# Performance work log

Hardware: AMD Instinct MI355X
Metric: run time of the kernel (lower is better)

Reference implementation:

```python
import jax, jax.numpy as jnp
import numpy as np

B, DX, DY = 128, 3, 3
D = DX * DY          # max_digit = 9
N = D * D            # num_nodes = 81
HID = 96
EMB = 16
ITERS = 4
M = B * N * D        # LSTM flattened rows = 93312


def _sudoku_adj():
    idx = np.arange(N)
    r, c = idx // D, idx % D
    br, bc = r // DX, c // DY
    same = (r[:, None] == r[None]) | (c[:, None] == c[None]) | ((br[:, None] == br[None]) & (bc[:, None] == bc[None]))
    return (same & ~np.eye(N, dtype=bool)).astype(np.float32)


def setup_inputs() -> dict:
    key = jax.random.key(0)
    ks = iter(jax.random.split(key, 40))

    def dense(shape, fan_in):
        return jax.random.normal(next(ks), shape, jnp.float32) / np.float32(np.sqrt(fan_in))

    return {
        "inputs": jax.random.randint(next(ks), (B, N), 0, D + 1, jnp.int32),
        "c0": jax.random.normal(next(ks), (M, HID), jnp.float32),
        "adj_cell": jnp.asarray((np.ones((D, D)) - np.eye(D)).astype(np.float32)),
        "adj_digit": jnp.asarray(_sudoku_adj()),
        "enc_W1": dense((3, EMB), 3), "enc_b1": jnp.zeros((EMB,), jnp.float32),
        "enc_W2": dense((EMB, HID), EMB), "enc_b2": jnp.zeros((HID,), jnp.float32),
        "cr_W": dense((3, HID, HID), HID), "cr_b": jnp.zeros((3, HID), jnp.float32),
        "dr_W": dense((3, HID, HID), HID), "dr_b": jnp.zeros((3, HID), jnp.float32),
        "gm_W1": dense((3 * HID, HID), 3 * HID), "gm_b1": jnp.zeros((HID,), jnp.float32),
        "gm_W2": dense((2, HID, HID), HID), "gm_b2": jnp.zeros((2, HID), jnp.float32),
        "lstm_Wih": dense((4 * HID, HID), HID), "lstm_Whh": dense((4 * HID, HID), HID),
        "lstm_bih": jnp.zeros((4 * HID,), jnp.float32), "lstm_bhh": jnp.zeros((4 * HID,), jnp.float32),
        "r_W12": dense((2, HID, HID), HID), "r_b12": jnp.zeros((2, HID), jnp.float32),
        "r_W3": dense((HID, 1), HID), "r_b3": jnp.zeros((1,), jnp.float32),
        "iters": ITERS,
    }


def _mlp(x, Ws, bs):
    # stacked MLP: ReLU between layers, none after the last
    L = Ws.shape[0]
    for l in range(L):
        x = x @ Ws[l] + bs[l]
        if l < L - 1:
            x = jax.nn.relu(x)
    return x


def _forward(inputs, c0, adj_cell, adj_digit, enc_W1, enc_b1, enc_W2, enc_b2,
             cr_W, cr_b, dr_W, dr_b, gm_W1, gm_b1, gm_W2, gm_b2,
             lstm_Wih, lstm_Whh, lstm_bih, lstm_bhh, r_W12, r_b12, r_W3, r_b3, iters):
    # mask: [B,N,D,3] = (blank, equals digit d+1, filled-with-other-digit)
    eq = inputs[:, :, None] == jnp.arange(1, D + 1, dtype=inputs.dtype)[None, None, :]
    given = inputs != 0
    mask = jnp.stack([
        jnp.broadcast_to((~given)[:, :, None], eq.shape), eq,
        (~eq) & given[:, :, None]
    ], axis=-1).astype(jnp.float32)

    X = jax.nn.relu(mask @ enc_W1 + enc_b1) @ enc_W2 + enc_b2  # [B,N,D,HID]

    def lstm_step(x, h, c):
        gates = x @ lstm_Wih.T + lstm_bih + h @ lstm_Whh.T + lstm_bhh
        i, f, g, o = jnp.split(gates, 4, axis=-1)  # PyTorch gate order i,f,g,o
        c = jax.nn.sigmoid(f) * c + jax.nn.sigmoid(i) * jnp.tanh(g)
        h = jax.nn.sigmoid(o) * jnp.tanh(c)
        return h, c

    def step(carry, _):
        h, c = carry  # [M,HID] each
        Hn = h.reshape(X.shape)
        # relational message passing: per-node MLP then sum over graph edges
        msg_cell = jnp.einsum('bndh,de->bneh', _mlp(Hn, cr_W, cr_b), adj_cell)
        msg_digit = jnp.einsum('bndh,nm->bmdh', _mlp(Hn, dr_W, dr_b), adj_digit)
        g = jnp.concatenate([X, msg_cell, msg_digit], axis=-1)  # [B,N,D,3*HID]
        g = jax.nn.relu(g @ gm_W1 + gm_b1)
        g = jax.nn.relu(g @ gm_W2[0] + gm_b2[0])
        g = g @ gm_W2[1] + gm_b2[1]
        h, c = lstm_step(g.reshape(-1, HID), h, c)
        Hn = h.reshape(X.shape)
        out = jax.nn.relu(Hn @ r_W12[0] + r_b12[0])
        out = jax.nn.relu(out @ r_W12[1] + r_b12[1])
        out = (out @ r_W3 + r_b3)[..., 0]  # [B,N,D]
        return (h, c), out

    (_, _), outs = jax.lax.scan(step, (X.reshape(-1, HID), c0), None, length=iters)
    return outs  # [iters,B,N,D]


def reference(inputs, c0, adj_cell, adj_digit, enc_W1, enc_b1, enc_W2, enc_b2,
              cr_W, cr_b, dr_W, dr_b, gm_W1, gm_b1, gm_W2, gm_b2,
              lstm_Wih, lstm_Whh, lstm_bih, lstm_bhh, r_W12, r_b12, r_W3, r_b3, iters):
    return _forward(inputs, c0, adj_cell, adj_digit, enc_W1, enc_b1, enc_W2, enc_b2,
                    cr_W, cr_b, dr_W, dr_b, gm_W1, gm_b1, gm_W2, gm_b2,
                    lstm_Wih, lstm_Whh, lstm_bih, lstm_bhh, r_W12, r_b12, r_W3, r_b3, iters)
```

## Files before the change

kernel.cpp:

```cpp
#include <hip/hip_runtime.h>
#include <hip/hip_bf16.h>

typedef unsigned short u16;
typedef __bf16 bf16x8 __attribute__((ext_vector_type(8)));
typedef float  f32x4  __attribute__((ext_vector_type(4)));
typedef u16    u16x8  __attribute__((ext_vector_type(8)));

#define HID   96
#define LDP   104
#define MROWS 93312
#define BN    10368
#define GRID_TILE 1458
#define FUSE_GRID 5832
#define SGX   100
#define PST   97
#define TBUF  1664
#define FST   520

#define FCH 9216

#define MFMA(a,b,c) __builtin_amdgcn_mfma_f32_16x16x32_bf16((a),(b),(c),0,0,0)

__device__ __forceinline__ float bf2f(u16 x){
  union { float f; unsigned u; } v; v.u = ((unsigned)x) << 16; return v.f;
}
__device__ __forceinline__ u16 f2bf(float f){
  union { __bf16 b; u16 u; } v; v.b = (__bf16)f; return v.u;
}
__device__ __forceinline__ float frcp(float x){ return __builtin_amdgcn_rcpf(x); }
__device__ __forceinline__ float sigf(float x){ return frcp(1.f + __expf(-x)); }
__device__ __forceinline__ float tanhf_(float x){
  float xx = fminf(fmaxf(x, -15.f), 15.f);
  float e = __expf(-2.f * xx);
  return (1.f - e) * frcp(1.f + e);
}
__device__ __forceinline__ void lds_fence(){
  asm volatile("s_waitcnt lgkmcnt(0)" ::: "memory");
}

struct Frags { bf16x8 a0, a1, a2; };

__device__ __forceinline__ Frags load_afrags_g(const u16* __restrict__ A, size_t row0, int lane){
  int t16 = lane & 15, q = lane >> 4;
  const u16* p = A + (row0 + (size_t)t16) * 96 + q * 8;
  Frags f;
  f.a0 = *reinterpret_cast<const bf16x8*>(p);
  f.a1 = *reinterpret_cast<const bf16x8*>(p + 32);
  f.a2 = *reinterpret_cast<const bf16x8*>(p + 64);
  return f;
}
__device__ __forceinline__ Frags load_afrags_s(const u16* sA, int row0, int lane){
  int t16 = lane & 15, q = lane >> 4;
  const u16* p = sA + (row0 + t16) * LDP + q * 8;
  Frags f;
  f.a0 = *reinterpret_cast<const bf16x8*>(p);
  f.a1 = *reinterpret_cast<const bf16x8*>(p + 32);
  f.a2 = *reinterpret_cast<const bf16x8*>(p + 64);
  return f;
}

__device__ __forceinline__ void layer_g(Frags f, const u16* __restrict__ wb,
    const float* __restrict__ bias, u16* dst, int dstStride, size_t rowBase,
    bool relu, int lane)
{
  int t16 = lane & 15, q = lane >> 4;
  #pragma unroll
  for (int nt = 0; nt < 6; nt++){
    float b = bias ? bias[nt * 16 + t16] : 0.f;
    f32x4 acc = {b, b, b, b};
    const u16* wp = wb + nt * 1536 + lane * 8;
    acc = MFMA(f.a0, *reinterpret_cast<const bf16x8*>(wp),        acc);
    acc = MFMA(f.a1, *reinterpret_cast<const bf16x8*>(wp + 512),  acc);
    acc = MFMA(f.a2, *reinterpret_cast<const bf16x8*>(wp + 1024), acc);
    #pragma unroll
    for (int j = 0; j < 4; j++){
      float v = acc[j];
      if (relu) v = fmaxf(v, 0.f);
      dst[(rowBase + q * 4 + j) * (size_t)dstStride + nt * 16 + t16] = f2bf(v);
    }
  }
}

__device__ __forceinline__ void layer_split(Frags f, const u16* __restrict__ wb,
    const float* __restrict__ bias, u16* dst, bool relu, int lane, int w)
{
  int t16 = lane & 15, q = lane >> 4;
  #pragma unroll
  for (int nt = w; nt < 6; nt += 4){
    float b = bias ? bias[nt * 16 + t16] : 0.f;
    f32x4 acc = {b, b, b, b};
    const u16* wp = wb + nt * 1536 + lane * 8;
    acc = MFMA(f.a0, *reinterpret_cast<const bf16x8*>(wp),        acc);
    acc = MFMA(f.a1, *reinterpret_cast<const bf16x8*>(wp + 512),  acc);
    acc = MFMA(f.a2, *reinterpret_cast<const bf16x8*>(wp + 1024), acc);
    #pragma unroll
    for (int j = 0; j < 4; j++){
      float v = acc[j];
      if (relu) v = fmaxf(v, 0.f);
      dst[(q * 4 + j) * LDP + nt * 16 + t16] = f2bf(v);
    }
  }
}

__device__ __forceinline__ void mfma6_g(f32x4* acc, Frags f,
    const u16* __restrict__ wb, int lane)
{
  #pragma unroll
  for (int jt = 0; jt < 6; jt++){
    const u16* wp = wb + jt * 1536 + lane * 8;
    acc[jt] = MFMA(f.a0, *reinterpret_cast<const bf16x8*>(wp),        acc[jt]);
    acc[jt] = MFMA(f.a1, *reinterpret_cast<const bf16x8*>(wp + 512),  acc[jt]);
    acc[jt] = MFMA(f.a2, *reinterpret_cast<const bf16x8*>(wp + 1024), acc[jt]);
  }
}

__global__ __launch_bounds__(256) void k_prep2(const float* __restrict__ crW,
    const float* __restrict__ drW, const float* __restrict__ gmW2,
    const float* __restrict__ rW12, const float* __restrict__ Whh,
    u16* __restrict__ pWB)
{
  int b = blockIdx.x, tid = threadIdx.x;
  if (b < 7){
    const float* src; int ch;
    if      (b == 0){ src = crW;          ch = 0;  }
    else if (b == 1){ src = crW  + 9216;  ch = 1;  }
    else if (b == 2){ src = drW;          ch = 3;  }
    else if (b == 3){ src = drW  + 9216;  ch = 4;  }
    else if (b == 4){ src = gmW2;         ch = 8;  }
    else if (b == 5){ src = rW12;         ch = 10; }
    else            { src = rW12 + 9216;  ch = 11; }
    u16* dst = pWB + ch * FCH;
    #pragma unroll
    for (int i = 0; i < 36; i++){
      int idx = tid + i * 256;
      int f = idx >> 9, rem = idx & 511, l = rem >> 3, j = rem & 7;
      int nt = f / 3, kc = f - nt * 3;
      int n = nt * 16 + (l & 15);
      int k = ((l >> 4) << 3) + kc * 32 + j;
      dst[idx] = f2bf(src[k * 96 + n]);
    }
  } else {
    int bb = b - 7;
    u16* dst = pWB + (16 + bb) * FCH;
    const float* src = Whh + bb * 9216;
    #pragma unroll
    for (int i = 0; i < 36; i++){
      int idx = tid + i * 256;
      int f = idx >> 9, rem = idx & 511, l = rem >> 3, j = rem & 7;
      int nt = f / 3, kc = f - nt * 3;
      int n = nt * 16 + (l & 15);
      int k = ((l >> 4) << 3) + kc * 32 + j;
      dst[idx] = f2bf(src[n * 96 + k]);
    }
  }
}

__global__ __launch_bounds__(256) void k_prepadj(u16* __restrict__ adjM)
{
  int tid = threadIdx.x;
  for (int i = tid; i < 9216; i += 256){
    int m = i / 96, n = i - (i / 96) * 96;
    float v = 0.f;
    if (m < 81 && n < 81 && m != n){
      int rm = m / 9, cm = m - rm * 9;
      int rn = n / 9, cn = n - rn * 9;
      if (rm == rn || cm == cn || ((rm / 3 == rn / 3) && (cm / 3 == cn / 3)))
        v = 1.f;
    }
    adjM[i] = f2bf(v);
  }
}

__global__ __launch_bounds__(256) void k_prepc(const float* __restrict__ crW,
    const float* __restrict__ crB, const float* __restrict__ drW,
    const float* __restrict__ drB, const float* __restrict__ gmW1,
    u16* __restrict__ pWB, float* __restrict__ bY, float* __restrict__ bZ)
{
  __shared__ float sM[96 * PST];
  __shared__ float sW[96 * PST];
  int b = blockIdx.x, g = b / 9, seg = b - g * 9, tid = threadIdx.x;
  const float* L = (g == 0 ? crW : drW) + 2 * 9216;
  const float* R = gmW1 + (g == 0 ? 9216 : 18432);
  for (int i = tid; i < 9216; i += 256){
    int r = i / 96, cc = i - r * 96;
    sM[r * PST + cc] = L[i];
    sW[r * PST + cc] = R[i];
  }
  __syncthreads();
  if (seg == 0){
    const float* bv = (g == 0 ? crB : drB) + 192;
    float* bo = (g == 0 ? bY : bZ);
    for (int n = tid; n < 96; n += 256){
      float a = 0.f;
      for (int j = 0; j < 96; j++) a += bv[j] * sW[j * PST + n];
      bo[n] = a;
    }
  }
  u16* dst = pWB + (g == 0 ? 2 : 5) * FCH;
  #pragma unroll
  for (int i = 0; i < 4; i++){
    int idx = seg * 1024 + tid + i * 256;
    int f = idx >> 9, rem = idx & 511, l = rem >> 3, j = rem & 7;
    int nt = f / 3, kc = f - nt * 3;
    int n = nt * 16 + (l & 15);
    int k = ((l >> 4) << 3) + kc * 32 + j;
    float a = 0.f;
    #pragma unroll 4
    for (int jj = 0; jj < 96; jj++) a += sM[k * PST + jj] * sW[jj * PST + n];
    dst[idx] = f2bf(a);
  }
}

__global__ __launch_bounds__(256) void k_prepf(const float* __restrict__ gmW2,
    const float* __restrict__ Wih, u16* __restrict__ pWB)
{
  __shared__ float sW[96 * PST];
  int b = blockIdx.x, g = b / 9, seg = b - g * 9, tid = threadIdx.x;
  for (int i = tid; i < 9216; i += 256){
    int r = i / 96, cc = i - r * 96;
    sW[r * PST + cc] = gmW2[9216 + i];
  }
  __syncthreads();
  u16* dst = pWB + (12 + g) * FCH;
  #pragma unroll
  for (int i = 0; i < 4; i++){
    int idx = seg * 1024 + tid + i * 256;
    int f = idx >> 9, rem = idx & 511, l = rem >> 3, j = rem & 7;
    int nt = f / 3, kc = f - nt * 3;
    int n = nt * 16 + (l & 15);
    int k = ((l >> 4) << 3) + kc * 32 + j;
    const float* wr = Wih + (g * 96 + n) * 96;
    float a = 0.f;
    #pragma unroll 4
    for (int jj = 0; jj < 96; jj++) a += sW[k * PST + jj] * wr[jj];
    dst[idx] = f2bf(a);
  }
}

__global__ void k_tables(const float* __restrict__ eW1, const float* __restrict__ eb1,
                         const float* __restrict__ eW2, const float* __restrict__ eb2,
                         const float* __restrict__ gmW1, const float* __restrict__ gmb1,
                         const float* __restrict__ bih, const float* __restrict__ bhh,
                         const float* __restrict__ gmb2, const float* __restrict__ Wih,
                         float* __restrict__ XTab, float* __restrict__ XgTab,
                         float* __restrict__ bsx)
{
  __shared__ float sX[3][96];
  int j = threadIdx.x;
  for (int n = j; n < 384; n += 128){
    float acc = bih[n] + bhh[n];
    const float* wr = Wih + n * 96;
    for (int jj = 0; jj < 96; jj++) acc += gmb2[96 + jj] * wr[jj];
    bsx[n] = acc;
  }
  if (j < 96){
    for (int ch = 0; ch < 3; ch++){
      float acc = eb2[j];
      for (int e = 0; e < 16; e++){
        float hv = fmaxf(eW1[ch * 16 + e] + eb1[e], 0.f);
        acc += hv * eW2[e * 96 + j];
      }
      sX[ch][j] = acc;
      XTab[ch * 96 + j] = acc;
    }
  }
  __syncthreads();
  if (j < 96){
    for (int ch = 0; ch < 3; ch++){
      float acc = gmb1[j];
      for (int k = 0; k < 96; k++) acc += sX[ch][k] * gmW1[k * 96 + j];
      XgTab[ch * 96 + j] = acc;
    }
  }
}

__global__ __launch_bounds__(256) void k_init(const int* __restrict__ inputs,
    const float* __restrict__ XTab, u16* __restrict__ h)
{
  int idx = blockIdx.x * 256 + threadIdx.x;
  int m = idx / 12, h8 = idx - m * 12;
  int bn = m / 9, d = m - bn * 9;
  int inp = inputs[bn];
  int ch = (inp == 0) ? 0 : ((inp == d + 1) ? 1 : 2);
  const float* xt = XTab + ch * 96 + h8 * 8;
  u16* hp = h + (size_t)m * 96 + h8 * 8;
  #pragma unroll
  for (int e = 0; e < 8; e++) hp[e] = f2bf(xt[e]);
}

__global__ __launch_bounds__(256) void k_ab3(const u16* __restrict__ h,
    u16* __restrict__ Y, u16* __restrict__ Z,
    const u16* __restrict__ pWB, const float* __restrict__ crB,
    const float* __restrict__ drB, const float* __restrict__ bY,
    const float* __restrict__ bZ)
{
  __shared__ u16 sA[64 * LDP];
  const int tid = threadIdx.x, lane = tid & 63, wave = tid >> 6;
  const int wrow = wave * 16;
  const size_t rbase = (size_t)blockIdx.x * 64;

  Frags hf = load_afrags_g(h, rbase + wrow, lane);

  layer_g(hf, pWB, crB, sA, LDP, wrow, true, lane);                  lds_fence();
  Frags f = load_afrags_s(sA, wrow, lane);
  layer_g(f, pWB + 1 * FCH, crB + 96, sA, LDP, wrow, true, lane);    lds_fence();
  f = load_afrags_s(sA, wrow, lane);
  layer_g(f, pWB + 2 * FCH, bY, Y, 96, rbase + wrow, false, lane);
  lds_fence();

  layer_g(hf, pWB + 3 * FCH, drB, sA, LDP, wrow, true, lane);        lds_fence();
  f = load_afrags_s(sA, wrow, lane);
  layer_g(f, pWB + 4 * FCH, drB + 96, sA, LDP, wrow, true, lane);    lds_fence();
  f = load_afrags_s(sA, wrow, lane);
  layer_g(f, pWB + 5 * FCH, bZ, Z, 96, rbase + wrow, false, lane);
}

__global__ __launch_bounds__(256) void k_msg(u16* __restrict__ Z,
    const u16* __restrict__ Y, u16* __restrict__ Ssum,
    const u16* __restrict__ adjM)
{
  __shared__ u16 sF[18 * FST];
  const int tid = threadIdx.x;
  if (blockIdx.x >= 1152){
    int idx = (blockIdx.x - 1152) * 256 + tid;
    int bn = idx / 12, h8 = idx - bn * 12;
    const u16* base = Y + (size_t)bn * 864 + h8 * 8;
    float s[8];
    #pragma unroll
    for (int e = 0; e < 8; e++) s[e] = 0.f;
    #pragma unroll
    for (int d = 0; d < 9; d++){
      u16x8 v = *reinterpret_cast<const u16x8*>(base + d * 96);
      #pragma unroll
      for (int e = 0; e < 8; e++) s[e] += bf2f(v[e]);
    }
    u16x8 o;
    #pragma unroll
    for (int e = 0; e < 8; e++) o[e] = f2bf(s[e]);
    *reinterpret_cast<u16x8*>(Ssum + (size_t)bn * 96 + h8 * 8) = o;
    return;
  }
  const int b = blockIdx.x / 9, d = blockIdx.x - b * 9;
  const size_t base = ((size_t)b * 729 + d) * 96;
  for (int i = tid; i < 1152; i += 256){
    int n = i / 12, k8 = i - (i / 12) * 12;
    u16x8 v;
    if (n < 81){
      v = *reinterpret_cast<const u16x8*>(Z + base + (size_t)n * 864 + k8 * 8);
    } else {
      for (int e = 0; e < 8; e++) v[e] = 0;
    }
    int f = (k8 >> 1) * 3 + (n >> 5);
    int lbase = ((n >> 3) & 3) * 16 + (k8 & 1) * 8;
    u16* p = sF + f * FST + lbase * 8 + (n & 7);
    #pragma unroll
    for (int e = 0; e < 8; e++) p[e * 8] = v[e];
  }
  __syncthreads();
  const int lane = tid & 63, w = tid >> 6;
  const int t16 = lane & 15, q = lane >> 4;
  #pragma unroll
  for (int ti = 0; ti < 9; ti++){
    int t = w + ti * 4;
    int mt = t / 6, nt = t - mt * 6;
    Frags fa = load_afrags_g(adjM, mt * 16, lane);
    f32x4 acc = {0.f, 0.f, 0.f, 0.f};
    const u16* bp = sF + nt * 3 * FST + lane * 8;
    acc = MFMA(fa.a0, *reinterpret_cast<const bf16x8*>(bp),           acc);
    acc = MFMA(fa.a1, *reinterpret_cast<const bf16x8*>(bp + FST),     acc);
    acc = MFMA(fa.a2, *reinterpret_cast<const bf16x8*>(bp + 2 * FST), acc);
    int c = nt * 16 + t16;
    #pragma unroll
    for (int jr = 0; jr < 4; jr++){
      int m = mt * 16 + q * 4 + jr;
      if (m < 81) Z[base + (size_t)m * 864 + c] = f2bf(acc[jr]);
    }
  }
}

__global__ __launch_bounds__(256, 4) void k_fuse16x(u16* Y, u16* Z,
    const u16* __restrict__ Ssum,
    const int* __restrict__ inputs, const float* __restrict__ XgTab,
    const u16* __restrict__ pWB, const float* __restrict__ gmb2,
    u16* h, const float* cin, float* cout,
    const float* __restrict__ bsx, const float* __restrict__ rb12,
    const float* __restrict__ rW3, const float* __restrict__ rb3,
    float* __restrict__ out, const float* __restrict__ crB,
    const float* __restrict__ drB, const float* __restrict__ bY,
    const float* __restrict__ bZ, int doAB)
{
  __shared__ u16 sA[16 * LDP];
  __shared__ u16 sU[6 * TBUF];
  u16*   sB   = sU;
  float* sGhF = reinterpret_cast<float*>(sU + TBUF);
  const int tid = threadIdx.x, lane = tid & 63, w = tid >> 6;
  const int t16 = lane & 15, q = lane >> 4;
  const size_t rbase = (size_t)blockIdx.x * 16;

  float cpre[6];
  #pragma unroll
  for (int e = 0; e < 6; e++){
    int idx = e * 256 + tid;
    int r = idx / 96, col = idx - r * 96;
    cpre[e] = cin[(rbase + r) * 96 + col];
  }
  Frags fh = load_afrags_g(h, rbase, lane);

  if (tid < 192){
    int rl = tid / 12, kc = tid - rl * 12;
    int m = (int)rbase + rl;
    int bn = m / 9, d = m - bn * 9;
    int inp = inputs[bn];
    int ch = (inp == 0) ? 0 : ((inp == d + 1) ? 1 : 2);
    const float* xg = XgTab + ch * 96 + kc * 8;
    u16x8 vy = *reinterpret_cast<const u16x8*>(Y    + (size_t)m * 96 + kc * 8);
    u16x8 vz = *reinterpret_cast<const u16x8*>(Z    + (size_t)m * 96 + kc * 8);
    u16x8 vs = *reinterpret_cast<const u16x8*>(Ssum + (size_t)bn * 96 + kc * 8);
    u16x8 o;
    #pragma unroll
    for (int e = 0; e < 8; e++)
      o[e] = f2bf(fmaxf(xg[e] + bf2f(vs[e]) - bf2f(vy[e]) + bf2f(vz[e]), 0.f));
    *reinterpret_cast<u16x8*>(sA + rl * LDP + kc * 8) = o;
  }
  __syncthreads();

  {
    Frags f = load_afrags_s(sA, 0, lane);
    layer_split(f, pWB + 8 * FCH, gmb2, sB, true, lane, w);
  }
  __syncthreads();

  f32x4 acc[6];
  #pragma unroll
  for (int nt = 0; nt < 6; nt++){
    float b = bsx[w * 96 + nt * 16 + t16];
    f32x4 a = {b, b, b, b};
    acc[nt] = a;
  }
  {
    Frags fa = load_afrags_s(sB, 0, lane);
    mfma6_g(acc, fa, pWB + (12 + w) * FCH, lane);
    mfma6_g(acc, fh, pWB + (16 + w) * FCH, lane);
  }

  if (q < 2){
    #pragma unroll
    for (int nt = 0; nt < 6; nt++)
      #pragma unroll
      for (int j = 0; j < 4; j++)
        sGhF[(w * 8 + q * 4 + j) * SGX + nt * 16 + t16] = acc[nt][j];
  }
  __syncthreads();
  #pragma unroll
  for (int e = 0; e < 3; e++){
    int idx = e * 256 + tid;
    int r = idx / 96, col = idx - r * 96;
    float iv = sGhF[(0 * 8 + r) * SGX + col];
    float fv = sGhF[(1 * 8 + r) * SGX + col];
    float gv = sGhF[(2 * 8 + r) * SGX + col];
    float ov = sGhF[(3 * 8 + r) * SGX + col];
    size_t m = rbase + r;
    float cn = sigf(fv) * cpre[e] + sigf(iv) * tanhf_(gv);
    float hn = sigf(ov) * tanhf_(cn);
    cout[m * 96 + col] = cn;
    u16 hb = f2bf(hn);
    h[m * 96 + col] = hb;
    sA[r * LDP + col] = hb;
  }
  __syncthreads();

  if (q >= 2){
    #pragma unroll
    for (int nt = 0; nt < 6; nt++)
      #pragma unroll
      for (int j = 0; j < 4; j++)
        sGhF[(w * 8 + (q - 2) * 4 + j) * SGX + nt * 16 + t16] = acc[nt][j];
  }
  __syncthreads();
  #pragma unroll
  for (int e = 0; e < 3; e++){
    int idx = (e + 3) * 256 + tid;
    int r = idx / 96, col = idx - r * 96;
    float iv = sGhF[(0 * 8 + r - 8) * SGX + col];
    float fv = sGhF[(1 * 8 + r - 8) * SGX + col];
    float gv = sGhF[(2 * 8 + r - 8) * SGX + col];
    float ov = sGhF[(3 * 8 + r - 8) * SGX + col];
    size_t m = rbase + r;
    float cn = sigf(fv) * cpre[e + 3] + sigf(iv) * tanhf_(gv);
    float hn = sigf(ov) * tanhf_(cn);
    cout[m * 96 + col] = cn;
    u16 hb = f2bf(hn);
    h[m * 96 + col] = hb;
    sA[r * LDP + col] = hb;
  }
  __syncthreads();

  if (w == 0){
    u16* bA = sU + 0 * TBUF;
    u16* bB = sU + 1 * TBUF;
    Frags f = load_afrags_s(sA, 0, lane);
    layer_g(f, pWB + 10 * FCH, rb12, bA, LDP, 0, true, lane);        lds_fence();
    f = load_afrags_s(bA, 0, lane);
    layer_g(f, pWB + 11 * FCH, rb12 + 96, bB, LDP, 0, true, lane);   lds_fence();
    int row = lane >> 2, part = lane & 3;
    float s = 0.f;
    const u16* rp = bB + row * LDP + part * 24;
    #pragma unroll
    for (int k = 0; k < 24; k++) s += bf2f(rp[k]) * rW3[part * 24 + k];
    s += __shfl_xor(s, 1);
    s += __shfl_xor(s, 2);
    if (part == 0) out[rbase + row] = s + rb3[0];
  } else if (w == 1 && doAB){
    u16* bA = sU + 2 * TBUF;
    u16* bB = sU + 3 * TBUF;
    Frags f = load_afrags_s(sA, 0, lane);
    layer_g(f, pWB + 0 * FCH, crB, bA, LDP, 0, true, lane);          lds_fence();
    f = load_afrags_s(bA, 0, lane);
    layer_g(f, pWB + 1 * FCH, crB + 96, bB, LDP, 0, true, lane);     lds_fence();
    f = load_afrags_s(bB, 0, lane);
    layer_g(f, pWB + 2 * FCH, bY, Y, 96, rbase, false, lane);
  } else if (w == 2 && doAB){
    u16* bA = sU + 4 * TBUF;
    u16* bB = sU + 5 * TBUF;
    Frags f = load_afrags_s(sA, 0, lane);
    layer_g(f, pWB + 3 * FCH, drB, bA, LDP, 0, true, lane);          lds_fence();
    f = load_afrags_s(bA, 0, lane);
    layer_g(f, pWB + 4 * FCH, drB + 96, bB, LDP, 0, true, lane);     lds_fence();
    f = load_afrags_s(bB, 0, lane);
    layer_g(f, pWB + 5 * FCH, bZ, Z, 96, rbase, false, lane);
  }
}

extern "C" void kernel_launch(void* const* d_in, const int* in_sizes, int n_in,
                              void* d_out, int out_size, void* d_ws, size_t ws_size,
                              hipStream_t stream)
{
  (void)in_sizes; (void)n_in; (void)out_size; (void)ws_size;
  const int*   inputs = (const int*)d_in[0];
  const float* c0     = (const float*)d_in[1];
  const float* eW1  = (const float*)d_in[4];
  const float* eb1  = (const float*)d_in[5];
  const float* eW2  = (const float*)d_in[6];
  const float* eb2  = (const float*)d_in[7];
  const float* crW  = (const float*)d_in[8];
  const float* crB  = (const float*)d_in[9];
  const float* drW  = (const float*)d_in[10];
  const float* drB  = (const float*)d_in[11];
  const float* gmW1 = (const float*)d_in[12];
  const float* gmb1 = (const float*)d_in[13];
  const float* gmW2 = (const float*)d_in[14];
  const float* gmb2 = (const float*)d_in[15];
  const float* Wih  = (const float*)d_in[16];
  const float* Whh  = (const float*)d_in[17];
  const float* bih  = (const float*)d_in[18];
  const float* bhh  = (const float*)d_in[19];
  const float* rW12 = (const float*)d_in[20];
  const float* rb12 = (const float*)d_in[21];
  const float* rW3  = (const float*)d_in[22];
  const float* rb3  = (const float*)d_in[23];

  char* ws = (char*)d_ws;
  float* XgTab = (float*)(ws);
  float* XTab  = (float*)(ws + 4096);
  float* bsx   = (float*)(ws + 6144);
  float* bY    = (float*)(ws + 7680);
  float* bZ    = (float*)(ws + 8064);
  u16*   pWB   = (u16*)(ws + 8704);
  u16* h  = (u16*)(ws + 409600);
  u16* B1 = h  + (size_t)MROWS * 96;
  u16* B2 = B1 + (size_t)MROWS * 96;
  float* c = (float*)(B2 + (size_t)MROWS * 96);
  u16* Ssum = (u16*)(c + (size_t)MROWS * 96);
  u16* adjM = Ssum + (size_t)BN * 96;
  float* out = (float*)d_out;

  k_prep2<<<11, 256, 0, stream>>>(crW, drW, gmW2, rW12, Whh, pWB);
  k_prepc<<<18, 256, 0, stream>>>(crW, crB, drW, drB, gmW1, pWB, bY, bZ);
  k_prepf<<<36, 256, 0, stream>>>(gmW2, Wih, pWB);
  k_prepadj<<<1, 256, 0, stream>>>(adjM);
  k_tables<<<1, 128, 0, stream>>>(eW1, eb1, eW2, eb2, gmW1, gmb1, bih, bhh,
                                  gmb2, Wih, XTab, XgTab, bsx);
  k_init<<<(MROWS * 12) / 256, 256, 0, stream>>>(inputs, XTab, h);
  k_ab3<<<GRID_TILE, 256, 0, stream>>>(h, B1, B2, pWB, crB, drB, bY, bZ);

  for (int it = 0; it < 4; ++it){
    const float* cin = (it == 0) ? c0 : c;
    k_msg<<<1152 + 486, 256, 0, stream>>>(B2, B1, Ssum, adjM);
    k_fuse16x<<<FUSE_GRID, 256, 0, stream>>>(B1, B2, Ssum, inputs, XgTab, pWB,
                                             gmb2, h, cin, c, bsx, rb12, rW3, rb3,
                                             out + (size_t)it * MROWS,
                                             crB, drB, bY, bZ, (it < 3) ? 1 : 0);
  }
}
```

Baseline: 627.4 us.

## Process two 16-row tiles per block in fused LSTM kernel

The fused gate-MLP/LSTM/readout kernel now handles 32 rows per block as two 16-row tiles, halving the grid. Weight fragments loaded from global memory can be reused across both tiles, and per-block setup is amortized. In exchange each block does more serialized work, uses more LDS and registers (two h fragment sets, twelve c values), and has fewer blocks to spread across CUs, so latency hiding may suffer.

```diff
diff --git a/kernel.cpp b/kernel.cpp
--- a/kernel.cpp
+++ b/kernel.cpp
@@ -11,7 +11,7 @@
 #define MROWS 93312
 #define BN    10368
 #define GRID_TILE 1458
-#define FUSE_GRID 5832
+#define FUSE_GRID 2916
 #define SGX   100
 #define PST   97
 #define TBUF  1664
@@ -378,7 +378,80 @@
   }
 }
 
-__global__ __launch_bounds__(256, 4) void k_fuse16x(u16* Y, u16* Z,
+__device__ __forceinline__ void lstm_tile(const u16* sBt, Frags fht,
+    float cp0, float cp1, float cp2, float cp3, float cp4, float cp5,
+    u16* sAt, float* sGhF, size_t r0, u16* h, float* cout,
+    const float* __restrict__ bsx, const u16* __restrict__ pWB,
+    int tid, int lane, int w, int t16, int q)
+{
+  f32x4 acc[6];
+  #pragma unroll
+  for (int nt = 0; nt < 6; nt++){
+    float b = bsx[w * 96 + nt * 16 + t16];
+    f32x4 a = {b, b, b, b};
+    acc[nt] = a;
+  }
+  {
+    Frags fa = load_afrags_s(sBt, 0, lane);
+    mfma6_g(acc, fa, pWB + (12 + w) * FCH, lane);
+    mfma6_g(acc, fht, pWB + (16 + w) * FCH, lane);
+  }
+  float cparr[6] = {cp0, cp1, cp2, cp3, cp4, cp5};
+
+  if (q < 2){
+    #pragma unroll
+    for (int nt = 0; nt < 6; nt++)
+      #pragma unroll
+      for (int j = 0; j < 4; j++)
+        sGhF[(w * 8 + q * 4 + j) * SGX + nt * 16 + t16] = acc[nt][j];
+  }
+  __syncthreads();
+  #pragma unroll
+  for (int e = 0; e < 3; e++){
+    int idx = e * 256 + tid;
+    int r = idx / 96, col = idx - r * 96;
+    float iv = sGhF[(0 * 8 + r) * SGX + col];
+    float fv = sGhF[(1 * 8 + r) * SGX + col];
+    float gv = sGhF[(2 * 8 + r) * SGX + col];
+    float ov = sGhF[(3 * 8 + r) * SGX + col];
+    size_t m = r0 + r;
+    float cn = sigf(fv) * cparr[e] + sigf(iv) * tanhf_(gv);
+    float hn = sigf(ov) * tanhf_(cn);
+    cout[m * 96 + col] = cn;
+    u16 hb = f2bf(hn);
+    h[m * 96 + col] = hb;
+    sAt[r * LDP + col] = hb;
+  }
+  __syncthreads();
+
+  if (q >= 2){
+    #pragma unroll
+    for (int nt = 0; nt < 6; nt++)
+      #pragma unroll
+      for (int j = 0; j < 4; j++)
+        sGhF[(w * 8 + (q - 2) * 4 + j) * SGX + nt * 16 + t16] = acc[nt][j];
+  }
+  __syncthreads();
+  #pragma unroll
+  for (int e = 0; e < 3; e++){
+    int idx = (e + 3) * 256 + tid;
+    int r = idx / 96, col = idx - r * 96;
+    float iv = sGhF[(0 * 8 + r - 8) * SGX + col];
+    float fv = sGhF[(1 * 8 + r - 8) * SGX + col];
+    float gv = sGhF[(2 * 8 + r - 8) * SGX + col];
+    float ov = sGhF[(3 * 8 + r - 8) * SGX + col];
+    size_t m = r0 + r;
+    float cn = sigf(fv) * cparr[e + 3] + sigf(iv) * tanhf_(gv);
+    float hn = sigf(ov) * tanhf_(cn);
+    cout[m * 96 + col] = cn;
+    u16 hb = f2bf(hn);
+    h[m * 96 + col] = hb;
+    sAt[r * LDP + col] = hb;
+  }
+  __syncthreads();
+}
+
+__global__ __launch_bounds__(256, 4) void k_fuse32(u16* Y, u16* Z,
     const u16* __restrict__ Ssum,
     const int* __restrict__ inputs, const float* __restrict__ XgTab,
     const u16* __restrict__ pWB, const float* __restrict__ gmb2,
@@ -389,145 +462,109 @@
     const float* __restrict__ drB, const float* __restrict__ bY,
     const float* __restrict__ bZ, int doAB)
 {
-  __shared__ u16 sA[16 * LDP];
+  __shared__ u16 sA[2 * 16 * LDP];
   __shared__ u16 sU[6 * TBUF];
-  u16*   sB   = sU;
-  float* sGhF = reinterpret_cast<float*>(sU + TBUF);
+  u16*   sB0  = sU;
+  u16*   sB1  = sU + TBUF;
+  float* sGhF = reinterpret_cast<float*>(sU + 2 * TBUF);
   const int tid = threadIdx.x, lane = tid & 63, w = tid >> 6;
   const int t16 = lane & 15, q = lane >> 4;
-  const size_t rbase = (size_t)blockIdx.x * 16;
-
-  float cpre[6];
+  const size_t rbase = (size_t)blockIdx.x * 32;
+
+  float cp[12];
   #pragma unroll
   for (int e = 0; e < 6; e++){
     int idx = e * 256 + tid;
     int r = idx / 96, col = idx - r * 96;
-    cpre[e] = cin[(rbase + r) * 96 + col];
-  }
-  Frags fh = load_afrags_g(h, rbase, lane);
-
-  if (tid < 192){
-    int rl = tid / 12, kc = tid - rl * 12;
-    int m = (int)rbase + rl;
-    int bn = m / 9, d = m - bn * 9;
-    int inp = inputs[bn];
-    int ch = (inp == 0) ? 0 : ((inp == d + 1) ? 1 : 2);
-    const float* xg = XgTab + ch * 96 + kc * 8;
-    u16x8 vy = *reinterpret_cast<const u16x8*>(Y    + (size_t)m * 96 + kc * 8);
-    u16x8 vz = *reinterpret_cast<const u16x8*>(Z    + (size_t)m * 96 + kc * 8);
-    u16x8 vs = *reinterpret_cast<const u16x8*>(Ssum + (size_t)bn * 96 + kc * 8);
-    u16x8 o;
-    #pragma unroll
-    for (int e = 0; e < 8; e++)
-      o[e] = f2bf(fmaxf(xg[e] + bf2f(vs[e]) - bf2f(vy[e]) + bf2f(vz[e]), 0.f));
-    *reinterpret_cast<u16x8*>(sA + rl * LDP + kc * 8) = o;
+    cp[e]     = cin[(rbase + r) * 96 + col];
+    cp[e + 6] = cin[(rbase + 16 + r) * 96 + col];
+  }
+  Frags fh0 = load_afrags_g(h, rbase, lane);
+  Frags fh1 = load_afrags_g(h, rbase + 16, lane);
+
+  #pragma unroll
+  for (int t = 0; t < 2; t++){
+    if (tid < 192){
+      int rl = tid / 12, kc = tid - (tid / 12) * 12;
+      int m = (int)rbase + t * 16 + rl;
+      int bn = m / 9, d = m - bn * 9;
+      int inp = inputs[bn];
+      int ch = (inp == 0) ? 0 : ((inp == d + 1) ? 1 : 2);
+      const float* xg = XgTab + ch * 96 + kc * 8;
+      u16x8 vy = *reinterpret_cast<const u16x8*>(Y    + (size_t)m * 96 + kc * 8);
+      u16x8 vz = *reinterpret_cast<const u16x8*>(Z    + (size_t)m * 96 + kc * 8);
+      u16x8 vs = *reinterpret_cast<const u16x8*>(Ssum + (size_t)bn * 96 + kc * 8);
+      u16x8 o;
+      #pragma unroll
+      for (int e = 0; e < 8; e++)
+        o[e] = f2bf(fmaxf(xg[e] + bf2f(vs[e]) - bf2f(vy[e]) + bf2f(vz[e]), 0.f));
+      *reinterpret_cast<u16x8*>(sA + t * 16 * LDP + rl * LDP + kc * 8) = o;
+    }
   }
   __syncthreads();
 
   {
     Frags f = load_afrags_s(sA, 0, lane);
-    layer_split(f, pWB + 8 * FCH, gmb2, sB, true, lane, w);
-  }
-  __syncthreads();
-
-  f32x4 acc[6];
-  #pragma unroll
-  for (int nt = 0; nt < 6; nt++){
-    float b = bsx[w * 96 + nt * 16 + t16];
-    f32x4 a = {b, b, b, b};
-    acc[nt] = a;
-  }
-  {
-    Frags fa = load_afrags_s(sB, 0, lane);
-    mfma6_g(acc, fa, pWB + (12 + w) * FCH, lane);
-    mfma6_g(acc, fh, pWB + (16 + w) * FCH, lane);
-  }
-
-  if (q < 2){
-    #pragma unroll
-    for (int nt = 0; nt < 6; nt++)
-      #pragma unroll
-      for (int j = 0; j < 4; j++)
-        sGhF[(w * 8 + q * 4 + j) * SGX + nt * 16 + t16] = acc[nt][j];
-  }
-  __syncthreads();
-  #pragma unroll
-  for (int e = 0; e < 3; e++){
-    int idx = e * 256 + tid;
-    int r = idx / 96, col = idx - r * 96;
-    float iv = sGhF[(0 * 8 + r) * SGX + col];
-    float fv = sGhF[(1 * 8 + r) * SGX + col];
-    float gv = sGhF[(2 * 8 + r) * SGX + col];
-    float ov = sGhF[(3 * 8 + r) * SGX + col];
-    size_t m = rbase + r;
-    float cn = sigf(fv) * cpre[e] + sigf(iv) * tanhf_(gv);
-    float hn = sigf(ov) * tanhf_(cn);
-    cout[m * 96 + col] = cn;
-    u16 hb = f2bf(hn);
-    h[m * 96 + col] = hb;
-    sA[r * LDP + col] = hb;
-  }
-  __syncthreads();
-
-  if (q >= 2){
-    #pragma unroll
-    for (int nt = 0; nt < 6; nt++)
-      #pragma unroll
-      for (int j = 0; j < 4; j++)
-        sGhF[(w * 8 + (q - 2) * 4 + j) * SGX + nt * 16 + t16] = acc[nt][j];
-  }
-  __syncthreads();
-  #pragma unroll
-  for (int e = 0; e < 3; e++){
-    int idx = (e + 3) * 256 + tid;
-    int r = idx / 96, col = idx - r * 96;
-    float iv = sGhF[(0 * 8 + r - 8) * SGX + col];
-    float fv = sGhF[(1 * 8 + r - 8) * SGX + col];
-    float gv = sGhF[(2 * 8 + r - 8) * SGX + col];
-    float ov = sGhF[(3 * 8 + r - 8) * SGX + col];
-    size_t m = rbase + r;
-    float cn = sigf(fv) * cpre[e + 3] + sigf(iv) * tanhf_(gv);
-    float hn = sigf(ov) * tanhf_(cn);
-    cout[m * 96 + col] = cn;
-    u16 hb = f2bf(hn);
-    h[m * 96 + col] = hb;
-    sA[r * LDP + col] = hb;
-  }
-  __syncthreads();
+    layer_split(f, pWB + 8 * FCH, gmb2, sB0, true, lane, w);
+    Frags g = load_afrags_s(sA + 16 * LDP, 0, lane);
+    layer_split(g, pWB + 8 * FCH, gmb2, sB1, true, lane, w);
+  }
+  __syncthreads();
+
+  lstm_tile(sB0, fh0, cp[0], cp[1], cp[2], cp[3], cp[4], cp[5],
+            sA, sGhF, rbase, h, cout, bsx, pWB, tid, lane, w, t16, q);
+  lstm_tile(sB1, fh1, cp[6], cp[7], cp[8], cp[9], cp[10], cp[11],
+            sA + 16 * LDP, sGhF, rbase + 16, h, cout, bsx, pWB,
+            tid, lane, w, t16, q);
 
   if (w == 0){
     u16* bA = sU + 0 * TBUF;
     u16* bB = sU + 1 * TBUF;
-    Frags f = load_afrags_s(sA, 0, lane);
-    layer_g(f, pWB + 10 * FCH, rb12, bA, LDP, 0, true, lane);        lds_fence();
-    f = load_afrags_s(bA, 0, lane);
-    layer_g(f, pWB + 11 * FCH, rb12 + 96, bB, LDP, 0, true, lane);   lds_fence();
-    int row = lane >> 2, part = lane & 3;
-    float s = 0.f;
-    const u16* rp = bB + row * LDP + part * 24;
-    #pragma unroll
-    for (int k = 0; k < 24; k++) s += bf2f(rp[k]) * rW3[part * 24 + k];
-    s += __shfl_xor(s, 1);
-    s += __shfl_xor(s, 2);
-    if (part == 0) out[rbase + row] = s + rb3[0];
+    #pragma unroll
+    for (int t = 0; t < 2; t++){
+      const u16* src = sA + t * 16 * LDP;
+      Frags f = load_afrags_s(src, 0, lane);
+      layer_g(f, pWB + 10 * FCH, rb12, bA, LDP, 0, true, lane);      lds_fence();
+      f = load_afrags_s(bA, 0, lane);
+      layer_g(f, pWB + 11 * FCH, rb12 + 96, bB, LDP, 0, true, lane); lds_fence();
+      int row = lane >> 2, part = lane & 3;
+      float s = 0.f;
+      const u16* rp = bB + row * LDP + part * 24;
+      #pragma unroll
+      for (int k = 0; k < 24; k++) s += bf2f(rp[k]) * rW3[part * 24 + k];
+      s += __shfl_xor(s, 1);
+      s += __shfl_xor(s, 2);
+      if (part == 0) out[rbase + t * 16 + row] = s + rb3[0];
+      lds_fence();
+    }
   } else if (w == 1 && doAB){
     u16* bA = sU + 2 * TBUF;
     u16* bB = sU + 3 * TBUF;
-    Frags f = load_afrags_s(sA, 0, lane);
-    layer_g(f, pWB + 0 * FCH, crB, bA, LDP, 0, true, lane);          lds_fence();
-    f = load_afrags_s(bA, 0, lane);
-    layer_g(f, pWB + 1 * FCH, crB + 96, bB, LDP, 0, true, lane);     lds_fence();
-    f = load_afrags_s(bB, 0, lane);
-    layer_g(f, pWB + 2 * FCH, bY, Y, 96, rbase, false, lane);
+    #pragma unroll
+    for (int t = 0; t < 2; t++){
+      const u16* src = sA + t * 16 * LDP;
+      Frags f = load_afrags_s(src, 0, lane);
+      layer_g(f, pWB + 0 * FCH, crB, bA, LDP, 0, true, lane);        lds_fence();
+      f = load_afrags_s(bA, 0, lane);
+      layer_g(f, pWB + 1 * FCH, crB + 96, bB, LDP, 0, true, lane);   lds_fence();
+      f = load_afrags_s(bB, 0, lane);
+      layer_g(f, pWB + 2 * FCH, bY, Y, 96, rbase + t * 16, false, lane);
+      lds_fence();
+    }
   } else if (w == 2 && doAB){
     u16* bA = sU + 4 * TBUF;
     u16* bB = sU + 5 * TBUF;
-    Frags f = load_afrags_s(sA, 0, lane);
-    layer_g(f, pWB + 3 * FCH, drB, bA, LDP, 0, true, lane);          lds_fence();
-    f = load_afrags_s(bA, 0, lane);
-    layer_g(f, pWB + 4 * FCH, drB + 96, bB, LDP, 0, true, lane);     lds_fence();
-    f = load_afrags_s(bB, 0, lane);
-    layer_g(f, pWB + 5 * FCH, bZ, Z, 96, rbase, false, lane);
+    #pragma unroll
+    for (int t = 0; t < 2; t++){
+      const u16* src = sA + t * 16 * LDP;
+      Frags f = load_afrags_s(src, 0, lane);
+      layer_g(f, pWB + 3 * FCH, drB, bA, LDP, 0, true, lane);        lds_fence();
+      f = load_afrags_s(bA, 0, lane);
+      layer_g(f, pWB + 4 * FCH, drB + 96, bB, LDP, 0, true, lane);   lds_fence();
+      f = load_afrags_s(bB, 0, lane);
+      layer_g(f, pWB + 5 * FCH, bZ, Z, 96, rbase + t * 16, false, lane);
+      lds_fence();
+    }
   }
 }
 
@@ -586,9 +623,9 @@
   for (int it = 0; it < 4; ++it){
     const float* cin = (it == 0) ? c0 : c;
     k_msg<<<1152 + 486, 256, 0, stream>>>(B2, B1, Ssum, adjM);
-    k_fuse16x<<<FUSE_GRID, 256, 0, stream>>>(B1, B2, Ssum, inputs, XgTab, pWB,
-                                             gmb2, h, cin, c, bsx, rb12, rW3, rb3,
-                                             out + (size_t)it * MROWS,
-                                             crB, drB, bY, bZ, (it < 3) ? 1 : 0);
-  }
-}
+    k_fuse32<<<FUSE_GRID, 256, 0, stream>>>(B1, B2, Ssum, inputs, XgTab, pWB,
+                                            gmb2, h, cin, c, bsx, rb12, rW3, rb3,
+                                            out + (size_t)it * MROWS,
+                                            crB, drB, bY, bZ, (it < 3) ? 1 : 0);
+  }
+}
```

Measured after the change: 880.2 us. 1.4x slower.
